# Optimization experiments

Measured on AMD Instinct MI355X. Metric: run time of the kernel, lower is better.

## Reference

```python
import jax, jax.numpy as jnp
import numpy as np
from jax import lax


def setup_inputs() -> dict:
    key = jax.random.key(0)
    x = jax.random.normal(key, (4, 8192, 3), dtype=jnp.float32)
    return {"x": x, "k": 16}


def reference(x, k):
    p = x[..., :3]                                  # (B, N, 3)
    # Brute-force KNN: squared euclidean distances (B, N, N)
    sq = jnp.sum(p * p, axis=-1)                    # (B, N)
    d2 = sq[:, :, None] + sq[:, None, :] - 2.0 * jnp.einsum('bnd,bmd->bnm', p, p)
    _, idx = lax.top_k(-d2, k)                      # (B, N, k), nearest (incl. self)
    # Gather neighbors per batch
    neighbors = jax.vmap(lambda pts, ids: pts[ids])(p, idx)   # (B, N, k, 3)
    mean = jnp.mean(neighbors, axis=2, keepdims=True)          # (B, N, 1, 3)
    diff = neighbors - mean                                    # (B, N, k, 3)
    # cov = mean_k (diff diff^T) over neighbors -> (B, N, 3, 3)
    cov = jnp.einsum('bnki,bnkj->bnij', diff, diff) / k
    ev = jnp.linalg.eigvalsh(cov)                  # ascending: (B, N, 3)
    lambda0 = ev[..., 2]
    lambda1 = ev[..., 1]
    return lambda0 / lambda1
```

## Files before the change

### kernel.cpp

```cpp
#include <hip/hip_runtime.h>
#include <math.h>

#define NB 4
#define NP 8192
#define KK 16
#define QPB 64
#define NPTS (NB * NP)

#define TSAMP 1024
#define TTCH 128
#define NTS 8
#define BCH 1024
#define NBCH 8
#define CAP 62
#define SROW 66
#define SCH (64 * SROW + 2)
#define KCH 17
#define KQS (NBCH * KCH + 1)
#define PADKEY 0xFFFFFFFFFFFFFFFFull
#define TAU_MARGIN 2.5e-4f

#define CSWAP_DESC(a, b) { float _lo = fminf(a, b); float _hi = fmaxf(a, b); a = _hi; b = _lo; }
#define CSWAP_ASC(a, b)  { float _lo = fminf(a, b); float _hi = fmaxf(a, b); a = _lo; b = _hi; }

__device__ __forceinline__ float ref_sq(float x, float y, float z) {
  return __fadd_rn(__fadd_rn(__fmul_rn(x, x), __fmul_rn(y, y)), __fmul_rn(z, z));
}

__device__ __forceinline__ float ref_d2q(float qx, float qy, float qz, float sqq,
                                         float4 c) {
  float dot = __fadd_rn(__fadd_rn(__fmul_rn(qx, c.x), __fmul_rn(qy, c.y)),
                        __fmul_rn(qz, c.z));
  float s = __fadd_rn(sqq, c.w);
  return __fmaf_rn(-2.0f, dot, s);
}

__device__ __forceinline__ float fast_d2(float qx, float qy, float qz, float sqq,
                                         float4 c) {
  float dot = __fmaf_rn(qz, c.z, __fmaf_rn(qy, c.y, __fmul_rn(qx, c.x)));
  float s = __fadd_rn(sqq, c.w);
  return __fmaf_rn(-2.0f, dot, s);
}

__device__ __forceinline__ unsigned int ord_f32(float d) {
  unsigned int b = __float_as_uint(d);
  return b ^ ((b >> 31) ? 0xFFFFFFFFu : 0x80000000u);
}

__device__ __forceinline__ double eigen_ratio_tail(
    float cxx, float cyy, float czz, float cxy, float cxz, float cyz,
    float k1) {
  double a   = (double)__fmul_rn(cxx, k1), b = (double)__fmul_rn(cyy, k1);
  double c2  = (double)__fmul_rn(czz, k1);
  double dxy = (double)__fmul_rn(cxy, k1), exz = (double)__fmul_rn(cxz, k1);
  double fyz = (double)__fmul_rn(cyz, k1);
  double qm = (a + b + c2) / 3.0;
  double p1 = dxy * dxy + exz * exz + fyz * fyz;
  double aa = a - qm, bb = b - qm, cc = c2 - qm;
  double p2 = aa * aa + bb * bb + cc * cc + 2.0 * p1;
  if (p2 <= 0.0) return 1.0;
  double p  = sqrt(p2 / 6.0);
  double ip = 1.0 / p;
  double b00 = aa * ip, b11 = bb * ip, b22 = cc * ip;
  double b01 = dxy * ip, b02 = exz * ip, b12 = fyz * ip;
  double detB = b00 * (b11 * b22 - b12 * b12)
              - b01 * (b01 * b22 - b12 * b02)
              + b02 * (b01 * b12 - b11 * b02);
  double r = 0.5 * detB;
  r = fmin(1.0, fmax(-1.0, r));
  const double dcl = 2.0 * r;
  float phif = acosf((float)r) * (1.0f / 3.0f);
  double y0 = 2.0 * (double)cosf(phif);
  double y2 = 2.0 * (double)cosf(phif + 2.0943951f);
#pragma unroll
  for (int it = 0; it < 3; ++it) {
    double g0 = 3.0 * (y0 * y0 - 1.0);
    if (fabs(g0) > 1e-4) y0 -= (y0 * y0 * y0 - 3.0 * y0 - dcl) / g0;
    double g2 = 3.0 * (y2 * y2 - 1.0);
    if (fabs(g2) > 1e-4) y2 -= (y2 * y2 * y2 - 3.0 * y2 - dcl) / g2;
  }
  double e0 = qm + p * y0;
  double e2v = qm + p * y2;
  double e1 = 3.0 * qm - e0 - e2v;
  return e0 / e1;
}

__device__ __forceinline__ void topk_update(float bd[KK], float d[8]) {
  CSWAP_DESC(d[0], d[1]) CSWAP_DESC(d[2], d[3]) CSWAP_DESC(d[4], d[5]) CSWAP_DESC(d[6], d[7])
  CSWAP_DESC(d[0], d[2]) CSWAP_DESC(d[1], d[3]) CSWAP_DESC(d[4], d[6]) CSWAP_DESC(d[5], d[7])
  CSWAP_DESC(d[1], d[2]) CSWAP_DESC(d[5], d[6])
  CSWAP_DESC(d[0], d[4]) CSWAP_DESC(d[1], d[5]) CSWAP_DESC(d[2], d[6]) CSWAP_DESC(d[3], d[7])
  CSWAP_DESC(d[2], d[4]) CSWAP_DESC(d[3], d[5])
  CSWAP_DESC(d[1], d[2]) CSWAP_DESC(d[3], d[4]) CSWAP_DESC(d[5], d[6])
#pragma unroll
  for (int i = 0; i < 8; ++i) bd[8 + i] = fminf(bd[8 + i], d[i]);
#pragma unroll
  for (int i = 0; i < 8; ++i)  CSWAP_ASC(bd[i], bd[i + 8])
#pragma unroll
  for (int i = 0; i < 4; ++i)  CSWAP_ASC(bd[i], bd[i + 4])
#pragma unroll
  for (int i = 8; i < 12; ++i) CSWAP_ASC(bd[i], bd[i + 4])
#pragma unroll
  for (int g = 0; g < 4; ++g) {
    CSWAP_ASC(bd[4 * g + 0], bd[4 * g + 2]) CSWAP_ASC(bd[4 * g + 1], bd[4 * g + 3])
    CSWAP_ASC(bd[4 * g + 0], bd[4 * g + 1]) CSWAP_ASC(bd[4 * g + 2], bd[4 * g + 3])
  }
}

__global__ void prep_kernel(const float* __restrict__ x,
                            float4* __restrict__ cand) {
  int i = blockIdx.x * 256 + threadIdx.x;
  if (i < NPTS) {
    float px = x[3 * i + 0], py = x[3 * i + 1], pz = x[3 * i + 2];
    cand[i] = make_float4(px, py, pz, ref_sq(px, py, pz));
  }
}

__global__ __launch_bounds__(512) void tau_stage_kernel(
    const float4* __restrict__ cand, float* __restrict__ tauArr) {
  __shared__ __align__(16) char smem[NTS * 64 * 17 * 4];
  float4* samp = (float4*)smem;
  float (*s_t)[64][17] = (float (*)[64][17])smem;
  const int tid   = threadIdx.x;
  const int lane  = tid & 63;
  const int w     = __builtin_amdgcn_readfirstlane(tid >> 6);
  const int group = blockIdx.x;
  const int batch = group >> 7;
  const int qbase = (group & 127) * QPB;
  const float4* __restrict__ Cb = cand + (size_t)batch * NP;

  const float4 q = Cb[qbase + lane];
  const float qx = q.x, qy = q.y, qz = q.z, sqq = q.w;

#pragma unroll
  for (int r = 0; r < TSAMP / 512; ++r)
    samp[r * 512 + tid] = Cb[r * 512 + tid];
  __syncthreads();

  float bdA[KK], bdB[KK];
#pragma unroll
  for (int t = 0; t < KK; ++t) { bdA[t] = 3.4e38f; bdB[t] = 3.4e38f; }

  const int j0 = w * TTCH;
  for (int jj = 0; jj < TTCH; jj += 16) {
    const float4* xp = samp + (j0 + jj);
    float4 c[16];
#pragma unroll
    for (int u = 0; u < 16; ++u) c[u] = xp[u];
    float dA[8], dB[8];
#pragma unroll
    for (int u = 0; u < 8; ++u) dA[u] = fast_d2(qx, qy, qz, sqq, c[u]);
#pragma unroll
    for (int u = 0; u < 8; ++u) dB[u] = fast_d2(qx, qy, qz, sqq, c[8 + u]);
    topk_update(bdA, dA);
    topk_update(bdB, dB);
  }
  topk_update(bdA, &bdB[0]);
  topk_update(bdA, &bdB[8]);
  __syncthreads();

#pragma unroll
  for (int t = 0; t < KK; ++t) s_t[w][lane][t] = bdA[t];
  __syncthreads();

  if (w == 0) {
    float md[KK];
#pragma unroll
    for (int t = 0; t < KK; ++t) md[t] = s_t[0][lane][t];
#pragma unroll
    for (int s2 = 1; s2 < NTS; ++s2) {
      float d[KK];
#pragma unroll
      for (int t = 0; t < KK; ++t) d[t] = s_t[s2][lane][t];
      topk_update(md, &d[0]);
      topk_update(md, &d[8]);
    }
    tauArr[batch * NP + qbase + lane] = md[KK - 1];
  }
}

__global__ __launch_bounds__(512) void filter_select_kernel(
    const float4* __restrict__ cand, const float* __restrict__ tauArr,
    float* __restrict__ out) {
  extern __shared__ __align__(16) char smem[];
  unsigned short* s_idx = (unsigned short*)smem;
  unsigned long long* keys = (unsigned long long*)smem;
  unsigned short* s_cnt = (unsigned short*)(smem + 70144);

  const int tid   = threadIdx.x;
  const int lane  = tid & 63;
  const int w     = __builtin_amdgcn_readfirstlane(tid >> 6);
  const int group = blockIdx.x;
  const int batch = group >> 7;
  const int qbase = (group & 127) * QPB;
  const float4* __restrict__ Cb = cand + (size_t)batch * NP;

  {
    const int j0 = w * BCH;
    const float tau = tauArr[batch * NP + qbase + lane] + TAU_MARGIN;
    const float4 q = Cb[qbase + lane];
    const float qx = q.x, qy = q.y, qz = q.z, sqq = q.w;

    unsigned short* Srow = &s_idx[w * SCH + lane * SROW];
    int cnt = 0;
    for (int jj = 0; jj < BCH; jj += 16) {
      const float4* xp = Cb + (j0 + jj);
      float4 c[16];
#pragma unroll
      for (int u = 0; u < 16; ++u) c[u] = xp[u];
#pragma unroll
      for (int u = 0; u < 16; ++u) {
        float d = fast_d2(qx, qy, qz, sqq, c[u]);
        if (d <= tau) {
          if (cnt < CAP) Srow[1 + cnt] = (unsigned short)(j0 + jj + u);
          ++cnt;
        }
      }
    }
    s_cnt[w * 64 + lane] = (unsigned short)cnt;
  }
  __syncthreads();

  const int qlq = tid >> 3;
  const int pch = tid & 7;
  unsigned long long slots[KK];
#pragma unroll
  for (int t = 0; t < KK; ++t) slots[t] = PADKEY;
  {
    const float4 qq = Cb[qbase + qlq];
    const float q2x = qq.x, q2y = qq.y, q2z = qq.z, sq2 = qq.w;
    const unsigned short* row = &s_idx[pch * SCH + qlq * SROW + 1];
    int cnl = (int)s_cnt[pch * 64 + qlq];
    if (cnl > CAP) cnl = CAP;
    for (int e = 0; e < cnl; e += 8) {
      unsigned long long kv[8];
#pragma unroll
      for (int u = 0; u < 8; ++u) {
        const bool ok = (e + u) < cnl;
        const int j = ok ? (int)row[e + u] : 0;
        const float dd = ref_d2q(q2x, q2y, q2z, sq2, Cb[j]);
        kv[u] = ok ? ((((unsigned long long)ord_f32(dd)) << 32) |
                      (unsigned int)j)
                   : PADKEY;
      }
#pragma unroll
      for (int u = 0; u < 8; ++u) {
        const unsigned long long k = kv[u];
        if (k < slots[KK - 1]) {
#pragma unroll
          for (int t = KK - 1; t >= 1; --t) {
            unsigned long long lo =
                (slots[t] < k) ? slots[t] : k;
            slots[t] = (slots[t - 1] > lo) ? slots[t - 1] : lo;
          }
          slots[0] = (slots[0] < k) ? slots[0] : k;
        }
      }
    }
  }
  __syncthreads();

#pragma unroll
  for (int t = 0; t < KK; ++t)
    keys[qlq * KQS + pch * KCH + t] = slots[t];
  __syncthreads();

  if (tid < QPB) {
    const int ql = tid;
    const int qg = batch * NP + qbase + ql;
    const float4 qq = Cb[qbase + ql];
    const float q2x = qq.x, q2y = qq.y, q2z = qq.z, sq2 = qq.w;

    int total = 0;
    bool fs = false;
#pragma unroll
    for (int p = 0; p < NBCH; ++p) {
      const int c = (int)s_cnt[p * 64 + ql];
      if (c > CAP) fs = true;
      total += c;
    }
    if (total < KK) fs = true;

    int mjr[KK];
    if (!fs) {
      const unsigned long long* kq = keys + ql * KQS;
      int head[NBCH];
#pragma unroll
      for (int p = 0; p < NBCH; ++p) head[p] = 0;
#pragma unroll
      for (int t = 0; t < KK; ++t) {
        unsigned long long best = PADKEY;
        int bp = 0;
#pragma unroll
        for (int p = 0; p < NBCH; ++p) {
          const unsigned long long k =
              (head[p] < KK) ? kq[p * KCH + head[p]] : PADKEY;
          if (k < best) { best = k; bp = p; }
        }
        head[bp]++;
        mjr[t] = (int)(best & 0xFFFFull);
      }
    } else {
      float md[KK];
#pragma unroll
      for (int t = 0; t < KK; ++t) { md[t] = 3.4e38f; mjr[t] = 0; }
      for (int j = 0; j < NP; ++j) {
        float d = ref_d2q(q2x, q2y, q2z, sq2, Cb[j]);
        if (d < md[KK - 1]) {
          bool c0 = d < md[0];
#pragma unroll
          for (int t = KK - 1; t >= 1; --t) {
            bool cl = d < md[t];
            bool cp = d < md[t - 1];
            float nv = fmaxf(md[t - 1], fminf(md[t], d));
            mjr[t] = cl ? (cp ? mjr[t - 1] : j) : mjr[t];
            md[t] = nv;
          }
          mjr[0] = c0 ? j : mjr[0];
          md[0] = fminf(md[0], d);
        }
      }
    }

    float4 pts[KK];
#pragma unroll
    for (int s = 0; s < KK; ++s) pts[s] = Cb[mjr[s]];

    float sx = 0.f, sy = 0.f, sz = 0.f;
#pragma unroll
    for (int s = 0; s < KK; ++s) {
      sx = __fadd_rn(sx, pts[s].x);
      sy = __fadd_rn(sy, pts[s].y);
      sz = __fadd_rn(sz, pts[s].z);
    }
    const float k1 = 1.0f / KK;
    const float mx = sx * k1, my = sy * k1, mz = sz * k1;

    float cxx = 0.f, cxy = 0.f, cxz = 0.f, cyy = 0.f, cyz = 0.f, czz = 0.f;
#pragma unroll
    for (int s = 0; s < KK; ++s) {
      float dx = __fsub_rn(pts[s].x, mx);
      float dy = __fsub_rn(pts[s].y, my);
      float dz = __fsub_rn(pts[s].z, mz);
      cxx = __fadd_rn(cxx, __fmul_rn(dx, dx));
      cxy = __fadd_rn(cxy, __fmul_rn(dx, dy));
      cxz = __fadd_rn(cxz, __fmul_rn(dx, dz));
      cyy = __fadd_rn(cyy, __fmul_rn(dy, dy));
      cyz = __fadd_rn(cyz, __fmul_rn(dy, dz));
      czz = __fadd_rn(czz, __fmul_rn(dz, dz));
    }

    out[qg] = (float)eigen_ratio_tail(cxx, cyy, czz, cxy, cxz, cyz, k1);
  }
}

__global__ __launch_bounds__(512, 4) void knn_eigen_fallback(
    const float4* __restrict__ cand, float* __restrict__ out) {
  __shared__ unsigned short s_j[8][QPB][18];

  const int tid   = threadIdx.x;
  const int lane  = tid & 63;
  const int w     = __builtin_amdgcn_readfirstlane(tid >> 6);
  const int batch = blockIdx.x >> 7;
  const int qbase = (blockIdx.x & 127) * QPB;
  const int FCH   = NP / 8;

  const float4* __restrict__ Cb = cand + (size_t)batch * NP;

  const float4 q = Cb[qbase + lane];
  const float qx = q.x, qy = q.y, qz = q.z, sqq = q.w;

  float bd[KK];
#pragma unroll
  for (int t = 0; t < KK; ++t) bd[t] = 3.4e38f;

  const int j0 = w * FCH;
  for (int jj = 0; jj < FCH; jj += 8) {
    const float4* xp = Cb + (j0 + jj);
    float4 c[8];
#pragma unroll
    for (int u = 0; u < 8; ++u) c[u] = xp[u];
    float d[8];
#pragma unroll
    for (int u = 0; u < 8; ++u) d[u] = ref_d2q(qx, qy, qz, sqq, c[u]);
    topk_update(bd, d);
  }

  const float T = bd[KK - 1];
  int cnt = 0;
  for (int jj = 0; jj < FCH; jj += 8) {
    const float4* xp = Cb + (j0 + jj);
    float4 c[8];
#pragma unroll
    for (int u = 0; u < 8; ++u) c[u] = xp[u];
#pragma unroll
    for (int u = 0; u < 8; ++u) {
      float d = ref_d2q(qx, qy, qz, sqq, c[u]);
      if (d <= T && cnt < KK) {
        s_j[w][lane][cnt] = (unsigned short)(j0 + jj + u);
        cnt++;
      }
    }
  }
  __syncthreads();

  if (tid < QPB) {
    const float4 qq = Cb[qbase + tid];
    const float q2x = qq.x, q2y = qq.y, q2z = qq.z, sq2 = qq.w;
    float md[KK]; int mj[KK];
#pragma unroll
    for (int t = 0; t < KK; ++t) { md[t] = 3.4e38f; mj[t] = 0; }
    for (int cch = 0; cch < 8; ++cch) {
      const unsigned int* rowp = (const unsigned int*)&s_j[cch][tid][0];
#pragma unroll
      for (int sp = 0; sp < KK / 2; ++sp) {
        unsigned int pk = rowp[sp];
#pragma unroll
        for (int half = 0; half < 2; ++half) {
          int j = (half == 0) ? (int)(pk & 0xFFFFu) : (int)(pk >> 16);
          float d = ref_d2q(q2x, q2y, q2z, sq2, Cb[j]);
          if (d < md[KK - 1]) {
            bool c0 = d < md[0];
#pragma unroll
            for (int t = KK - 1; t >= 1; --t) {
              bool cl = d < md[t];
              bool cp = d < md[t - 1];
              float nv = fmaxf(md[t - 1], fminf(md[t], d));
              mj[t] = cl ? (cp ? mj[t - 1] : j) : mj[t];
              md[t] = nv;
            }
            mj[0] = c0 ? j : mj[0];
            md[0] = fminf(md[0], d);
          }
        }
      }
    }
    float sx = 0.f, sy = 0.f, sz = 0.f;
#pragma unroll
    for (int s = 0; s < KK; ++s) {
      float4 pp = Cb[mj[s]];
      sx = __fadd_rn(sx, pp.x);
      sy = __fadd_rn(sy, pp.y);
      sz = __fadd_rn(sz, pp.z);
    }
    const float k1 = 1.0f / KK;
    const float mx = sx * k1, my = sy * k1, mz = sz * k1;
    float cxx = 0.f, cxy = 0.f, cxz = 0.f, cyy = 0.f, cyz = 0.f, czz = 0.f;
#pragma unroll
    for (int s = 0; s < KK; ++s) {
      float4 pp = Cb[mj[s]];
      float dx = __fsub_rn(pp.x, mx);
      float dy = __fsub_rn(pp.y, my);
      float dz = __fsub_rn(pp.z, mz);
      cxx = __fadd_rn(cxx, __fmul_rn(dx, dx));
      cxy = __fadd_rn(cxy, __fmul_rn(dx, dy));
      cxz = __fadd_rn(cxz, __fmul_rn(dx, dz));
      cyy = __fadd_rn(cyy, __fmul_rn(dy, dy));
      cyz = __fadd_rn(cyz, __fmul_rn(dy, dz));
      czz = __fadd_rn(czz, __fmul_rn(dz, dz));
    }
    out[(size_t)batch * NP + qbase + tid] =
        (float)eigen_ratio_tail(cxx, cyy, czz, cxy, cxz, cyz, k1);
  }
}

extern "C" void kernel_launch(void* const* d_in, const int* in_sizes, int n_in,
                              void* d_out, int out_size, void* d_ws, size_t ws_size,
                              hipStream_t stream) {
  const float* x = (const float*)d_in[0];
  float* out = (float*)d_out;
  float4* cand = (float4*)d_ws;
  float* tauArr = (float*)((char*)d_ws + (size_t)NPTS * sizeof(float4));
  const size_t need = (size_t)NPTS * sizeof(float4) +
                      (size_t)NPTS * sizeof(float);

  prep_kernel<<<dim3(NPTS / 256), dim3(256), 0, stream>>>(x, cand);
  if (ws_size >= need) {
    tau_stage_kernel<<<dim3(512), dim3(512), 0, stream>>>(cand, tauArr);
    const size_t fs_lds = 70144 + 1024;
    filter_select_kernel<<<dim3(512), dim3(512), fs_lds, stream>>>(
        cand, tauArr, out);
  } else {
    knn_eigen_fallback<<<dim3(NPTS / QPB), dim3(512), 0, stream>>>(cand, out);
  }
}
```

Baseline: 186.4 us.

## Fuse tau estimation stage into filter-select kernel

Merges the tau-sampling kernel into the filter/select kernel so that each block computes its queries' distance threshold in LDS and uses it directly, with no global tauArr round trip and one fewer launch. The sample buffer and partial top-k scratch reuse the filter kernel's LDS region, and the candidate loads are split into two 8-wide halves to lower register pressure. Launch bounds now request 4 waves per SIMD, which may force register spilling in the larger fused kernel.

```diff
diff --git a/kernel.cpp b/kernel.cpp
--- a/kernel.cpp
+++ b/kernel.cpp
@@ -9,7 +9,6 @@
 
 #define TSAMP 1024
 #define TTCH 128
-#define NTS 8
 #define BCH 1024
 #define NBCH 8
 #define CAP 62
@@ -116,11 +115,16 @@
   }
 }
 
-__global__ __launch_bounds__(512) void tau_stage_kernel(
-    const float4* __restrict__ cand, float* __restrict__ tauArr) {
-  __shared__ __align__(16) char smem[NTS * 64 * 17 * 4];
+__global__ __launch_bounds__(512, 4) void filter_select_kernel(
+    const float4* __restrict__ cand, float* __restrict__ out) {
+  extern __shared__ __align__(16) char smem[];
   float4* samp = (float4*)smem;
-  float (*s_t)[64][17] = (float (*)[64][17])smem;
+  float (*s_t)[64][17] = (float (*)[64][17])(smem + 16384);
+  unsigned short* s_idx = (unsigned short*)smem;
+  unsigned long long* keys = (unsigned long long*)smem;
+  unsigned short* s_cnt = (unsigned short*)(smem + 70144);
+  float* s_tau = (float*)(smem + 71168);
+
   const int tid   = threadIdx.x;
   const int lane  = tid & 63;
   const int w     = __builtin_amdgcn_readfirstlane(tid >> 6);
@@ -137,30 +141,39 @@
     samp[r * 512 + tid] = Cb[r * 512 + tid];
   __syncthreads();
 
-  float bdA[KK], bdB[KK];
-#pragma unroll
-  for (int t = 0; t < KK; ++t) { bdA[t] = 3.4e38f; bdB[t] = 3.4e38f; }
-
-  const int j0 = w * TTCH;
-  for (int jj = 0; jj < TTCH; jj += 16) {
-    const float4* xp = samp + (j0 + jj);
-    float4 c[16];
-#pragma unroll
-    for (int u = 0; u < 16; ++u) c[u] = xp[u];
-    float dA[8], dB[8];
-#pragma unroll
-    for (int u = 0; u < 8; ++u) dA[u] = fast_d2(qx, qy, qz, sqq, c[u]);
-#pragma unroll
-    for (int u = 0; u < 8; ++u) dB[u] = fast_d2(qx, qy, qz, sqq, c[8 + u]);
-    topk_update(bdA, dA);
-    topk_update(bdB, dB);
-  }
-  topk_update(bdA, &bdB[0]);
-  topk_update(bdA, &bdB[8]);
-  __syncthreads();
-
-#pragma unroll
-  for (int t = 0; t < KK; ++t) s_t[w][lane][t] = bdA[t];
+  {
+    float bdA[KK], bdB[KK];
+#pragma unroll
+    for (int t = 0; t < KK; ++t) { bdA[t] = 3.4e38f; bdB[t] = 3.4e38f; }
+
+    const int j0 = w * TTCH;
+    for (int jj = 0; jj < TTCH; jj += 16) {
+      float dA[8], dB[8];
+      {
+        const float4* xp = samp + (j0 + jj);
+        float4 c[8];
+#pragma unroll
+        for (int u = 0; u < 8; ++u) c[u] = xp[u];
+#pragma unroll
+        for (int u = 0; u < 8; ++u) dA[u] = fast_d2(qx, qy, qz, sqq, c[u]);
+      }
+      {
+        const float4* xp = samp + (j0 + jj + 8);
+        float4 c[8];
+#pragma unroll
+        for (int u = 0; u < 8; ++u) c[u] = xp[u];
+#pragma unroll
+        for (int u = 0; u < 8; ++u) dB[u] = fast_d2(qx, qy, qz, sqq, c[u]);
+      }
+      topk_update(bdA, dA);
+      topk_update(bdB, dB);
+    }
+    topk_update(bdA, &bdB[0]);
+    topk_update(bdA, &bdB[8]);
+
+#pragma unroll
+    for (int t = 0; t < KK; ++t) s_t[w][lane][t] = bdA[t];
+  }
   __syncthreads();
 
   if (w == 0) {
@@ -168,39 +181,20 @@
 #pragma unroll
     for (int t = 0; t < KK; ++t) md[t] = s_t[0][lane][t];
 #pragma unroll
-    for (int s2 = 1; s2 < NTS; ++s2) {
+    for (int s2 = 1; s2 < NBCH; ++s2) {
       float d[KK];
 #pragma unroll
       for (int t = 0; t < KK; ++t) d[t] = s_t[s2][lane][t];
       topk_update(md, &d[0]);
       topk_update(md, &d[8]);
     }
-    tauArr[batch * NP + qbase + lane] = md[KK - 1];
-  }
-}
-
-__global__ __launch_bounds__(512) void filter_select_kernel(
-    const float4* __restrict__ cand, const float* __restrict__ tauArr,
-    float* __restrict__ out) {
-  extern __shared__ __align__(16) char smem[];
-  unsigned short* s_idx = (unsigned short*)smem;
-  unsigned long long* keys = (unsigned long long*)smem;
-  unsigned short* s_cnt = (unsigned short*)(smem + 70144);
-
-  const int tid   = threadIdx.x;
-  const int lane  = tid & 63;
-  const int w     = __builtin_amdgcn_readfirstlane(tid >> 6);
-  const int group = blockIdx.x;
-  const int batch = group >> 7;
-  const int qbase = (group & 127) * QPB;
-  const float4* __restrict__ Cb = cand + (size_t)batch * NP;
+    s_tau[lane] = md[KK - 1];
+  }
+  __syncthreads();
 
   {
     const int j0 = w * BCH;
-    const float tau = tauArr[batch * NP + qbase + lane] + TAU_MARGIN;
-    const float4 q = Cb[qbase + lane];
-    const float qx = q.x, qy = q.y, qz = q.z, sqq = q.w;
-
+    const float tau = s_tau[lane] + TAU_MARGIN;
     unsigned short* Srow = &s_idx[w * SCH + lane * SROW];
     int cnt = 0;
     for (int jj = 0; jj < BCH; jj += 16) {
@@ -470,16 +464,12 @@
   const float* x = (const float*)d_in[0];
   float* out = (float*)d_out;
   float4* cand = (float4*)d_ws;
-  float* tauArr = (float*)((char*)d_ws + (size_t)NPTS * sizeof(float4));
-  const size_t need = (size_t)NPTS * sizeof(float4) +
-                      (size_t)NPTS * sizeof(float);
+  const size_t need = (size_t)NPTS * sizeof(float4);
 
   prep_kernel<<<dim3(NPTS / 256), dim3(256), 0, stream>>>(x, cand);
   if (ws_size >= need) {
-    tau_stage_kernel<<<dim3(512), dim3(512), 0, stream>>>(cand, tauArr);
-    const size_t fs_lds = 70144 + 1024;
-    filter_select_kernel<<<dim3(512), dim3(512), fs_lds, stream>>>(
-        cand, tauArr, out);
+    const size_t fs_lds = 71424;
+    filter_select_kernel<<<dim3(512), dim3(512), fs_lds, stream>>>(cand, out);
   } else {
     knn_eigen_fallback<<<dim3(NPTS / QPB), dim3(512), 0, stream>>>(cand, out);
   }
```

New measurement: 184.7 us. About the same (-0.9%).
